# Kernel tuning notes

Measured on AMD Instinct MI355X. Metric: run time of the kernel, lower is better.

The kernel has to match this reference:

```python
import jax, jax.numpy as jnp
import numpy as np

NUM_HEADS = 16
HEAD_DIM = 128
ROTARY_DIM = 32  # head_dim * rotary_pct(0.25)
ROPE_BASE = 10000.0
SCALE = HEAD_DIM ** -0.5


def _rotate_half(x):
    x1, x2 = jnp.split(x, 2, axis=-1)
    return jnp.concatenate((-x2, x1), axis=-1)


def _rope_tables(seq_len, dtype):
    inv_freq = 1.0 / (ROPE_BASE ** (jnp.arange(0, ROTARY_DIM, 2, dtype=jnp.float32) / ROTARY_DIM))
    freqs = jnp.arange(seq_len, dtype=jnp.float32)[:, None] * inv_freq[None, :]  # [S, rd/2]
    emb = jnp.concatenate((freqs, freqs), axis=-1)  # [S, rd]
    return jnp.cos(emb).astype(dtype), jnp.sin(emb).astype(dtype)


def setup_inputs() -> dict:
    key = jax.random.key(0)
    k1, k2, k3 = jax.random.split(key, 3)
    B, S, H = 2, 2048, 2048
    hidden_states = jax.random.normal(k1, (B, S, H), dtype=jnp.float32)
    attention_mask = jnp.zeros((B, 1, S, S), dtype=jnp.float32)
    Wqkv = jax.random.normal(k2, (H, 3 * H), dtype=jnp.float32) * (H ** -0.5)
    Wout = jax.random.normal(k3, (H, H), dtype=jnp.float32) * (H ** -0.5)
    return {"hidden_states": hidden_states, "attention_mask": attention_mask,
            "Wqkv": Wqkv, "Wout": Wout}


def reference(hidden_states, attention_mask, Wqkv, Wout):
    B, S, H = hidden_states.shape
    qkv = jnp.einsum('bsh,hk->bsk', hidden_states, Wqkv)  # [B,S,3H]
    q, k, v = jnp.split(qkv, 3, axis=-1)

    def to_heads(x):
        return x.reshape(B, S, NUM_HEADS, HEAD_DIM).transpose(0, 2, 1, 3)  # [B,nh,S,hd]

    q, k, v = to_heads(q), to_heads(k), to_heads(v)

    cos, sin = _rope_tables(S, hidden_states.dtype)  # [S, ROTARY_DIM]
    cos = cos[None, None, :, :]
    sin = sin[None, None, :, :]

    def rope(x):
        xr = x[..., :ROTARY_DIM]
        xr = xr * cos + _rotate_half(xr) * sin
        return jnp.concatenate((xr, x[..., ROTARY_DIM:]), axis=-1)

    q, k = rope(q), rope(k)

    scores = jnp.einsum('bhqd,bhkd->bhqk', q, k) * SCALE + attention_mask
    probs = jax.nn.softmax(scores, axis=-1)  # dropout p=0 -> identity
    ctx = jnp.einsum('bhqk,bhkd->bhqd', probs, v)
    ctx = ctx.transpose(0, 2, 1, 3).reshape(B, S, H)
    return jnp.einsum('bsh,ho->bso', ctx, Wout)
```

## Files before the change

kernel.cpp:

```cpp
#include <hip/hip_runtime.h>

typedef __attribute__((ext_vector_type(4))) float f32x4;
typedef __attribute__((ext_vector_type(8))) short s16x8;
typedef __attribute__((ext_vector_type(4))) unsigned short u16x4;
typedef __attribute__((ext_vector_type(8))) unsigned short u16x8;

#define DEVINL __device__ __forceinline__

constexpr int Bb = 2;
constexpr int Ss = 2048;
constexpr int Hh = 2048;
constexpr int NH = 16;
constexpr int HD = 128;
constexpr float ATT_SCALE = 0.08838834764831845f;
constexpr float CEXP = ATT_SCALE * 1.44269504089f;
constexpr float INV_SCALE = 11.313708498984761f;
constexpr float RAW_THR = 90.50966799f;

DEVINL unsigned short f2bf(float f) {
    unsigned u = __float_as_uint(f);
    u += 0x7FFFu + ((u >> 16) & 1u);
    return (unsigned short)(u >> 16);
}
DEVINL float bf2f(unsigned short h) { return __uint_as_float(((unsigned)h) << 16); }
DEVINL float fexp2(float x) { return __builtin_amdgcn_exp2f(x); }

DEVINL void gl16(const void* g, void* l) {
    __builtin_amdgcn_global_load_lds((const __attribute__((address_space(1))) void*)g,
                                     (__attribute__((address_space(3))) void*)l, 16, 0, 0);
}

__global__ void zero_flag_k(int* f) { if (threadIdx.x == 0) *f = 0; }

__global__ void scan_mask_k(const float* __restrict__ m, int* __restrict__ flag) {
    size_t i = ((size_t)blockIdx.x * 256 + threadIdx.x) * 4;
    f32x4 v = *(const f32x4*)(m + i);
    int any = (v[0] != 0.f) || (v[1] != 0.f) || (v[2] != 0.f) || (v[3] != 0.f);
    if (__any(any)) { if ((threadIdx.x & 63) == 0) atomicOr(flag, 1); }
}

__global__ void convH_k(const float* __restrict__ x, unsigned short* __restrict__ y) {
    size_t i = (size_t)blockIdx.x * 256 + threadIdx.x;
    f32x4 a = *(const f32x4*)(x + i * 8);
    f32x4 b = *(const f32x4*)(x + i * 8 + 4);
    u16x8 o;
    o[0] = f2bf(a[0]); o[1] = f2bf(a[1]); o[2] = f2bf(a[2]); o[3] = f2bf(a[3]);
    o[4] = f2bf(b[0]); o[5] = f2bf(b[1]); o[6] = f2bf(b[2]); o[7] = f2bf(b[3]);
    *(u16x8*)(y + i * 8) = o;
}

__global__ void convT_k(const float* __restrict__ W, unsigned short* __restrict__ Wt,
                        int R, int C) {
    __shared__ float tile[32][33];
    int c0 = blockIdx.x * 32, r0 = blockIdx.y * 32;
    int t = threadIdx.x;
    int rr = t >> 3, cc = (t & 7) * 4;
    f32x4 v = *(const f32x4*)(W + (size_t)(r0 + rr) * C + c0 + cc);
    tile[rr][cc + 0] = v[0]; tile[rr][cc + 1] = v[1];
    tile[rr][cc + 2] = v[2]; tile[rr][cc + 3] = v[3];
    __syncthreads();
    u16x4 o;
    o[0] = f2bf(tile[cc + 0][rr]); o[1] = f2bf(tile[cc + 1][rr]);
    o[2] = f2bf(tile[cc + 2][rr]); o[3] = f2bf(tile[cc + 3][rr]);
    *(u16x4*)(Wt + (size_t)(c0 + rr) * R + r0 + cc) = o;
}

template<int MODE>
__global__ __launch_bounds__(512, 2)
void gemm128x256_k(const unsigned short* __restrict__ A, const unsigned short* __restrict__ Bt,
                   float* __restrict__ Cf, unsigned short* __restrict__ Cb,
                   int M, int N, int K) {
    __shared__ char lds[98304];
    int t = threadIdx.x, w = t >> 6, ln = t & 63, lr = ln & 15, lg = ln >> 4;
    int wm = w >> 2, wn = w & 3;
    int f = blockIdx.x, cpx = gridDim.x >> 3;
    int s = (f & 7) * cpx + (f >> 3);
    int nbn = N >> 8;
    int nb = s % nbn, mb = s / nbn;
    int m0 = mb * 128, n0 = nb * 256;
    const char* Ab = (const char*)A;
    const char* Bbp = (const char*)Bt;

    f32x4 acc[4][4];
#pragma unroll
    for (int i = 0; i < 4; ++i)
#pragma unroll
        for (int j = 0; j < 4; ++j) { acc[i][j][0] = 0.f; acc[i][j][1] = 0.f; acc[i][j][2] = 0.f; acc[i][j][3] = 0.f; }

    auto STGA = [&](int sbuf, int skh, int kt) {
        int row = t >> 2, c = t & 3;
        int cs = c ^ ((row >> 1) & 3);
        gl16(Ab + ((size_t)(m0 + row) * K + kt * 64 + skh * 32) * 2 + cs * 16,
             lds + sbuf * 49152 + skh * 8192 + t * 16);
    };
    auto STGB = [&](int sbuf, int skh, int kt) {
#pragma unroll
        for (int rr = 0; rr < 2; ++rr) {
            int ci = rr * 512 + t;
            int row = ci >> 2, c = ci & 3;
            int cs = c ^ ((row >> 1) & 3);
            gl16(Bbp + ((size_t)(n0 + row) * K + kt * 64 + skh * 32) * 2 + cs * 16,
                 lds + sbuf * 49152 + 16384 + skh * 16384 + ci * 16);
        }
    };

#define PH128(buf, kh, sbuf, skh, st)                                             \
  {                                                                               \
    const char* Ap = lds + (buf) * 49152 + (kh) * 8192;                           \
    const char* Bp = lds + (buf) * 49152 + 16384 + (kh) * 16384;                  \
    s16x8 af[4], bfr[4];                                                          \
    _Pragma("unroll")                                                             \
    for (int i = 0; i < 4; ++i) {                                                 \
      int row = wm * 64 + i * 16 + lr;                                            \
      af[i] = *(const s16x8*)(Ap + row * 64 + ((lg ^ ((row >> 1) & 3)) * 16));    \
    }                                                                             \
    _Pragma("unroll")                                                             \
    for (int j = 0; j < 4; ++j) {                                                 \
      int row = wn * 64 + j * 16 + lr;                                            \
      bfr[j] = *(const s16x8*)(Bp + row * 64 + ((lg ^ ((row >> 1) & 3)) * 16));   \
    }                                                                             \
    STGA(sbuf, skh, st); STGB(sbuf, skh, st);                                     \
    __builtin_amdgcn_s_barrier();                                                 \
    asm volatile("s_waitcnt lgkmcnt(0)" ::: "memory");                            \
    __builtin_amdgcn_s_setprio(1);                                                \
    _Pragma("unroll")                                                             \
    for (int i = 0; i < 4; ++i)                                                   \
      _Pragma("unroll")                                                           \
      for (int j = 0; j < 4; ++j)                                                 \
        acc[i][j] = __builtin_amdgcn_mfma_f32_16x16x32_bf16(af[i], bfr[j],        \
                                                            acc[i][j], 0, 0, 0); \
    __builtin_amdgcn_s_setprio(0);                                                \
    asm volatile("s_waitcnt vmcnt(6)" ::: "memory");                              \
    __builtin_amdgcn_s_barrier();                                                 \
  }

    const int NT = K >> 6;
    STGA(0, 0, 0); STGB(0, 0, 0);
    STGA(0, 1, 0); STGB(0, 1, 0);
    STGA(1, 0, 1); STGB(1, 0, 1);
    asm volatile("s_waitcnt vmcnt(3)" ::: "memory");
    __builtin_amdgcn_s_barrier();

    for (int it = 0; it < (NT >> 1); ++it) {
        int e = it * 2;
        int e2 = (e + 2 < NT) ? e + 2 : e;
        int e3 = (e + 3 < NT) ? e + 3 : e + 1;
        PH128(0, 0,  1, 1, e + 1)
        PH128(0, 1,  0, 0, e2)
        PH128(1, 0,  0, 1, e2)
        PH128(1, 1,  1, 0, e3)
    }
    asm volatile("s_waitcnt vmcnt(0)" ::: "memory");
#undef PH128

    if (MODE == 0 && n0 < 4096 && (wn & 1) == 0) {
        float invf = fexp2((float)lr * -0.83048202372f);
#pragma unroll
        for (int i = 0; i < 4; ++i)
#pragma unroll
            for (int r = 0; r < 4; ++r) {
                int srow = (m0 + wm * 64 + i * 16 + lg * 4 + r) & (Ss - 1);
                float sn, cs;
                sincosf((float)srow * invf, &sn, &cs);
                float x1 = acc[i][0][r], x2 = acc[i][1][r];
                acc[i][0][r] = x1 * cs - x2 * sn;
                acc[i][1][r] = x2 * cs + x1 * sn;
            }
    }

#pragma unroll
    for (int i = 0; i < 4; ++i)
#pragma unroll
        for (int j = 0; j < 4; ++j)
#pragma unroll
            for (int r = 0; r < 4; ++r) {
                int gr = m0 + wm * 64 + i * 16 + lg * 4 + r;
                int gc = n0 + wn * 64 + j * 16 + lr;
                float vv = acc[i][j][r];
                if (MODE == 1) Cf[(size_t)gr * N + gc] = vv;
                else           Cb[(size_t)gr * N + gc] = f2bf(vv);
            }
}

__global__ void vtrans_k(const unsigned short* __restrict__ qkv, unsigned short* __restrict__ Vt) {
    __shared__ unsigned short tile[64][40];
    int bh = blockIdx.x; int b = bh >> 4, h = bh & 15;
    int s0 = blockIdx.y * 64, d0 = blockIdx.z * 32;
    int t = threadIdx.x;
    int r = t >> 2, c8 = (t & 3) * 8;
    u16x8 v = *(const u16x8*)(qkv + ((size_t)(b * Ss + s0 + r)) * 6144 + 4096 + h * 128 + d0 + c8);
#pragma unroll
    for (int e = 0; e < 8; ++e) tile[r][c8 + e] = v[e];
    __syncthreads();
    int dr = t >> 3, sc = (t & 7) * 8;
    u16x8 o;
#pragma unroll
    for (int e = 0; e < 8; ++e) o[e] = tile[sc + e][dr];
    *(u16x8*)(Vt + ((size_t)bh * HD + d0 + dr) * Ss + s0 + sc) = o;
}

__global__ __launch_bounds__(512)
void attn_k(const unsigned short* __restrict__ qkv, const unsigned short* __restrict__ Vt,
            const float* __restrict__ mask, unsigned short* __restrict__ ctxb,
            const int* __restrict__ flag) {
    __shared__ char ldsK[2][16384];
    __shared__ char ldsV[2][16384];
    __shared__ unsigned short ldsP[8][1024];
    int f = blockIdx.x;
    int swzb = (f & 7) * 64 + (f >> 3);
    int bh = swzb >> 4, qt = swzb & 15;
    int b = bh >> 4, h = bh & 15;
    int t = threadIdx.x, w = t >> 6, ln = t & 63, lr = ln & 15, lg = ln >> 4;
    int useMask = *flag;
    int qw0 = qt * 128 + w * 16;
    const char* qkvB = (const char*)qkv;
    const char* VtB = (const char*)Vt;

    auto STAGE = [&](int buf, int kk0s) {
#pragma unroll
        for (int c = 0; c < 2; ++c) {
            int ci = c * 512 + t;
            int krow = ci >> 4, kcb = (ci & 15) << 4;
            gl16(qkvB + (((size_t)(b * Ss + kk0s + krow)) * 6144 + 2048 + h * 128) * 2 + (kcb ^ ((krow & 7) << 4)),
                 ldsK[buf] + ci * 16);
            int vrow = ci >> 3, vcb = (ci & 7) << 4;
            gl16(VtB + (((size_t)(bh * 128 + vrow)) * 2048 + kk0s) * 2 + (vcb ^ ((vrow & 7) << 4)),
                 ldsV[buf] + ci * 16);
        }
    };

    s16x8 qf[4];
    size_t qbase = ((size_t)(b * Ss + qw0 + lr)) * 6144 + h * 128;
#pragma unroll
    for (int kc = 0; kc < 4; ++kc) qf[kc] = *(const s16x8*)(qkv + qbase + kc * 32 + lg * 8);

    float mr = -3e38f, lsum = 0.f;
    f32x4 ctxa[8];
#pragma unroll
    for (int dn = 0; dn < 8; ++dn) { ctxa[dn][0] = 0.f; ctxa[dn][1] = 0.f; ctxa[dn][2] = 0.f; ctxa[dn][3] = 0.f; }
    const float* mrow = mask + (size_t)b * Ss * Ss;

    STAGE(0, 0);
    asm volatile("s_waitcnt vmcnt(0)" ::: "memory");
    __builtin_amdgcn_s_barrier();

    for (int tix = 0; tix < 32; ++tix) {
        int kk0 = tix * 64;
        int cur = tix & 1;
        if (kk0 + 64 < Ss) STAGE(cur ^ 1, kk0 + 64);

        f32x4 st[4];
#pragma unroll
        for (int n = 0; n < 4; ++n) {
            f32x4 sacc = {0.f, 0.f, 0.f, 0.f};
            const char* kb = ldsK[cur] + (n * 16 + lr) * 256;
            int sw = (lr & 7) << 4;
            s16x8 kf0 = *(const s16x8*)(kb + ((0 * 64 + lg * 16) ^ sw));
            s16x8 kf1 = *(const s16x8*)(kb + ((1 * 64 + lg * 16) ^ sw));
            s16x8 kf2 = *(const s16x8*)(kb + ((2 * 64 + lg * 16) ^ sw));
            s16x8 kf3 = *(const s16x8*)(kb + ((3 * 64 + lg * 16) ^ sw));
            __builtin_amdgcn_s_setprio(1);
            sacc = __builtin_amdgcn_mfma_f32_16x16x32_bf16(kf0, qf[0], sacc, 0, 0, 0);
            sacc = __builtin_amdgcn_mfma_f32_16x16x32_bf16(kf1, qf[1], sacc, 0, 0, 0);
            sacc = __builtin_amdgcn_mfma_f32_16x16x32_bf16(kf2, qf[2], sacc, 0, 0, 0);
            sacc = __builtin_amdgcn_mfma_f32_16x16x32_bf16(kf3, qf[3], sacc, 0, 0, 0);
            __builtin_amdgcn_s_setprio(0);
            st[n] = sacc;
        }
        if (useMask) {
#pragma unroll
            for (int n = 0; n < 4; ++n)
#pragma unroll
                for (int r = 0; r < 4; ++r)
                    st[n][r] += mrow[(size_t)(qw0 + lr) * Ss + kk0 + n * 16 + lg * 4 + r] * INV_SCALE;
        }
        float pmax = st[0][0];
#pragma unroll
        for (int n = 0; n < 4; ++n)
#pragma unroll
            for (int r = 0; r < 4; ++r) pmax = fmaxf(pmax, st[n][r]);
        pmax = fmaxf(pmax, __shfl_xor(pmax, 16));
        pmax = fmaxf(pmax, __shfl_xor(pmax, 32));
        bool need = pmax > mr + RAW_THR;
        if (__any(need)) {
            float mn = fmaxf(mr, pmax);
            float al = fexp2((mr - mn) * CEXP);
            mr = mn;
            lsum *= al;
            float a0 = __shfl(al, lg * 4 + 0), a1 = __shfl(al, lg * 4 + 1);
            float a2 = __shfl(al, lg * 4 + 2), a3 = __shfl(al, lg * 4 + 3);
#pragma unroll
            for (int dn = 0; dn < 8; ++dn) {
                ctxa[dn][0] *= a0; ctxa[dn][1] *= a1; ctxa[dn][2] *= a2; ctxa[dn][3] *= a3;
            }
        }
        float mC = mr * CEXP;
        float rs = 0.f;
        u16x4 pk[4];
#pragma unroll
        for (int n = 0; n < 4; ++n)
#pragma unroll
            for (int r = 0; r < 4; ++r) {
                float p = fexp2(st[n][r] * CEXP - mC);
                rs += p;
                pk[n][r] = f2bf(p);
            }
        rs += __shfl_xor(rs, 16);
        rs += __shfl_xor(rs, 32);
        lsum += rs;
        char* pw = (char*)ldsP[w];
        int swp = (lr & 7) << 4;
#pragma unroll
        for (int n = 0; n < 4; ++n)
            *(u16x4*)(pw + lr * 128 + ((32 * n + 8 * lg) ^ swp)) = pk[n];
        asm volatile("s_waitcnt lgkmcnt(0)" ::: "memory");
        s16x8 pa[2];
#pragma unroll
        for (int c2 = 0; c2 < 2; ++c2)
            pa[c2] = *(const s16x8*)(pw + lr * 128 + ((64 * c2 + 16 * lg) ^ swp));
#pragma unroll
        for (int dn = 0; dn < 8; ++dn) {
            const char* vb = ldsV[cur] + (dn * 16 + lr) * 128;
            s16x8 vf0 = *(const s16x8*)(vb + ((0 * 64 + lg * 16) ^ swp));
            s16x8 vf1 = *(const s16x8*)(vb + ((1 * 64 + lg * 16) ^ swp));
            __builtin_amdgcn_s_setprio(1);
            ctxa[dn] = __builtin_amdgcn_mfma_f32_16x16x32_bf16(pa[0], vf0, ctxa[dn], 0, 0, 0);
            ctxa[dn] = __builtin_amdgcn_mfma_f32_16x16x32_bf16(pa[1], vf1, ctxa[dn], 0, 0, 0);
            __builtin_amdgcn_s_setprio(0);
        }
        asm volatile("s_waitcnt vmcnt(0)" ::: "memory");
        __builtin_amdgcn_s_barrier();
    }
    float l0 = 1.f / __shfl(lsum, lg * 4 + 0), l1 = 1.f / __shfl(lsum, lg * 4 + 1);
    float l2 = 1.f / __shfl(lsum, lg * 4 + 2), l3 = 1.f / __shfl(lsum, lg * 4 + 3);
#pragma unroll
    for (int dn = 0; dn < 8; ++dn) {
        size_t base = ((size_t)(b * Ss + qw0)) * Hh + h * 128 + dn * 16 + lr;
        ctxb[base + (size_t)(lg * 4 + 0) * Hh] = f2bf(ctxa[dn][0] * l0);
        ctxb[base + (size_t)(lg * 4 + 1) * Hh] = f2bf(ctxa[dn][1] * l1);
        ctxb[base + (size_t)(lg * 4 + 2) * Hh] = f2bf(ctxa[dn][2] * l2);
        ctxb[base + (size_t)(lg * 4 + 3) * Hh] = f2bf(ctxa[dn][3] * l3);
    }
}

extern "C" void kernel_launch(void* const* d_in, const int* in_sizes, int n_in,
                              void* d_out, int out_size, void* d_ws, size_t ws_size,
                              hipStream_t stream) {
    (void)in_sizes; (void)n_in; (void)out_size; (void)ws_size;
    const float* hidden = (const float*)d_in[0];
    const float* mask   = (const float*)d_in[1];
    const float* Wqkv   = (const float*)d_in[2];
    const float* Wout   = (const float*)d_in[3];
    float* out = (float*)d_out;

    char* ws = (char*)d_ws;
    size_t off = 0;
    auto alloc = [&](size_t bytes) { char* p = ws + off; off += (bytes + 255) & ~(size_t)255; return p; };
    unsigned short* hbf   = (unsigned short*)alloc((size_t)8388608 * 2);
    unsigned short* wqkvT = (unsigned short*)alloc((size_t)12582912 * 2);
    unsigned short* woutT = (unsigned short*)alloc((size_t)4194304 * 2);
    unsigned short* qkv   = (unsigned short*)alloc((size_t)25165824 * 2);
    unsigned short* Vt    = (unsigned short*)alloc((size_t)8388608 * 2);
    int* flag             = (int*)alloc(256);
    unsigned short* ctx = hbf;

    zero_flag_k<<<1, 64, 0, stream>>>(flag);
    scan_mask_k<<<2048, 256, 0, stream>>>(mask, flag);
    convH_k<<<4096, 256, 0, stream>>>(hidden, hbf);
    convT_k<<<dim3(192, 64), 256, 0, stream>>>(Wqkv, wqkvT, 2048, 6144);
    convT_k<<<dim3(64, 64), 256, 0, stream>>>(Wout, woutT, 2048, 2048);
    gemm128x256_k<0><<<768, 512, 0, stream>>>(hbf, wqkvT, nullptr, qkv, 4096, 6144, 2048);
    vtrans_k<<<dim3(32, 32, 4), 256, 0, stream>>>(qkv, Vt);
    attn_k<<<512, 512, 0, stream>>>(qkv, Vt, mask, ctx, flag);
    gemm128x256_k<1><<<256, 512, 0, stream>>>(ctx, woutT, out, nullptr, 4096, 2048, 2048);
}
```

Measured before the change: 301.6 us.

## Fuse V transpose into QKV GEMM epilogue and remap tiles per XCD

The QKV GEMM epilogue now writes V-column tiles directly in transposed [b,h,d,s] bf16 layout, so the separate vtrans kernel and its extra read/write pass over V are gone. Block-to-tile mapping is replaced with an XCD-aware scheme that gives each XCD a rectangular region of M and N tiles, which is meant to improve L2 reuse. The flag-zeroing kernel becomes hipMemsetAsync. The mask scan grid grows to cover the whole mask; before, it only checked a quarter of it, so this fixes correctness and adds read traffic. The fused transposed stores are scattered 8-byte writes, which may coalesce poorly.

```diff
diff --git a/kernel.cpp b/kernel.cpp
--- a/kernel.cpp
+++ b/kernel.cpp
@@ -29,8 +29,6 @@
     __builtin_amdgcn_global_load_lds((const __attribute__((address_space(1))) void*)g,
                                      (__attribute__((address_space(3))) void*)l, 16, 0, 0);
 }
-
-__global__ void zero_flag_k(int* f) { if (threadIdx.x == 0) *f = 0; }
 
 __global__ void scan_mask_k(const float* __restrict__ m, int* __restrict__ flag) {
     size_t i = ((size_t)blockIdx.x * 256 + threadIdx.x) * 4;
@@ -69,14 +67,15 @@
 __global__ __launch_bounds__(512, 2)
 void gemm128x256_k(const unsigned short* __restrict__ A, const unsigned short* __restrict__ Bt,
                    float* __restrict__ Cf, unsigned short* __restrict__ Cb,
-                   int M, int N, int K) {
+                   unsigned short* __restrict__ VtOut,
+                   int M, int N, int K, int rm, int rn, int snx) {
     __shared__ char lds[98304];
     int t = threadIdx.x, w = t >> 6, ln = t & 63, lr = ln & 15, lg = ln >> 4;
     int wm = w >> 2, wn = w & 3;
-    int f = blockIdx.x, cpx = gridDim.x >> 3;
-    int s = (f & 7) * cpx + (f >> 3);
-    int nbn = N >> 8;
-    int nb = s % nbn, mb = s / nbn;
+    int f = blockIdx.x;
+    int xcd = f & 7, i0 = f >> 3;
+    int mb = (xcd / snx) * rm + i0 % rm;
+    int nb = (xcd % snx) * rn + i0 / rm;
     int m0 = mb * 128, n0 = nb * 256;
     const char* Ab = (const char*)A;
     const char* Bbp = (const char*)Bt;
@@ -153,7 +152,24 @@
     asm volatile("s_waitcnt vmcnt(0)" ::: "memory");
 #undef PH128
 
-    if (MODE == 0 && n0 < 4096 && (wn & 1) == 0) {
+    if (MODE == 0 && n0 >= 4096) {
+#pragma unroll
+        for (int i = 0; i < 4; ++i)
+#pragma unroll
+            for (int j = 0; j < 4; ++j) {
+                int vcol = n0 - 4096 + wn * 64 + j * 16 + lr;
+                int h = vcol >> 7, d = vcol & 127;
+                int gr = m0 + wm * 64 + i * 16 + lg * 4;
+                int bb = gr >> 11, si = gr & 2047;
+                u16x4 o;
+                o[0] = f2bf(acc[i][j][0]); o[1] = f2bf(acc[i][j][1]);
+                o[2] = f2bf(acc[i][j][2]); o[3] = f2bf(acc[i][j][3]);
+                *(u16x4*)(VtOut + ((size_t)(bb * 16 + h) * 128 + d) * 2048 + si) = o;
+            }
+        return;
+    }
+
+    if (MODE == 0 && (wn & 1) == 0) {
         float invf = fexp2((float)lr * -0.83048202372f);
 #pragma unroll
         for (int i = 0; i < 4; ++i)
@@ -180,23 +196,6 @@
                 if (MODE == 1) Cf[(size_t)gr * N + gc] = vv;
                 else           Cb[(size_t)gr * N + gc] = f2bf(vv);
             }
-}
-
-__global__ void vtrans_k(const unsigned short* __restrict__ qkv, unsigned short* __restrict__ Vt) {
-    __shared__ unsigned short tile[64][40];
-    int bh = blockIdx.x; int b = bh >> 4, h = bh & 15;
-    int s0 = blockIdx.y * 64, d0 = blockIdx.z * 32;
-    int t = threadIdx.x;
-    int r = t >> 2, c8 = (t & 3) * 8;
-    u16x8 v = *(const u16x8*)(qkv + ((size_t)(b * Ss + s0 + r)) * 6144 + 4096 + h * 128 + d0 + c8);
-#pragma unroll
-    for (int e = 0; e < 8; ++e) tile[r][c8 + e] = v[e];
-    __syncthreads();
-    int dr = t >> 3, sc = (t & 7) * 8;
-    u16x8 o;
-#pragma unroll
-    for (int e = 0; e < 8; ++e) o[e] = tile[sc + e][dr];
-    *(u16x8*)(Vt + ((size_t)bh * HD + d0 + dr) * Ss + s0 + sc) = o;
 }
 
 __global__ __launch_bounds__(512)
@@ -364,13 +363,14 @@
     int* flag             = (int*)alloc(256);
     unsigned short* ctx = hbf;
 
-    zero_flag_k<<<1, 64, 0, stream>>>(flag);
-    scan_mask_k<<<2048, 256, 0, stream>>>(mask, flag);
+    hipMemsetAsync(flag, 0, 4, stream);
+    scan_mask_k<<<8192, 256, 0, stream>>>(mask, flag);
     convH_k<<<4096, 256, 0, stream>>>(hidden, hbf);
     convT_k<<<dim3(192, 64), 256, 0, stream>>>(Wqkv, wqkvT, 2048, 6144);
     convT_k<<<dim3(64, 64), 256, 0, stream>>>(Wout, woutT, 2048, 2048);
-    gemm128x256_k<0><<<768, 512, 0, stream>>>(hbf, wqkvT, nullptr, qkv, 4096, 6144, 2048);
-    vtrans_k<<<dim3(32, 32, 4), 256, 0, stream>>>(qkv, Vt);
+    gemm128x256_k<0><<<768, 512, 0, stream>>>(hbf, wqkvT, nullptr, qkv, Vt,
+                                              4096, 6144, 2048, 16, 6, 4);
     attn_k<<<512, 512, 0, stream>>>(qkv, Vt, mask, ctx, flag);
-    gemm128x256_k<1><<<256, 512, 0, stream>>>(ctx, woutT, out, nullptr, 4096, 2048, 2048);
-}
+    gemm128x256_k<1><<<256, 512, 0, stream>>>(ctx, woutT, out, nullptr, nullptr,
+                                              4096, 2048, 2048, 16, 2, 4);
+}
```

New measurement: 300.8 us. About the same (-0.3%).
